# Kernel optimization log

Hardware: AMD Instinct MI355X
Metric: run time of the kernel (lower is better)

Reference implementation:

```python
import jax, jax.numpy as jnp
import numpy as np

HEAD_DIM = 64
CLIP = 64  # clipping_distance
B, S = 32, 1024


def setup_inputs() -> dict:
    key = jax.random.key(0)
    kq, kk, kv, km, kt = jax.random.split(key, 5)
    q = jax.random.normal(kq, (B, S, HEAD_DIM), dtype=jnp.float32)
    k = jax.random.normal(kk, (B, S, HEAD_DIM), dtype=jnp.float32)
    v = jax.random.normal(kv, (B, S, HEAD_DIM), dtype=jnp.float32)
    mask = jax.random.randint(km, (B, S, S), 0, 2).astype(jnp.bool_)
    pos_table = jax.random.normal(kt, (2 * CLIP + 1, HEAD_DIM), dtype=jnp.float32)
    return {"q": q, "k": k, "v": v, "mask": mask, "pos_table": pos_table}


def reference(q, k, v, mask, pos_table):
    scaling = 1.0 / np.sqrt(HEAD_DIM).astype(np.float32)
    Sq, Sk = q.shape[1], k.shape[1]
    # relative positions k_idx - q_idx, clipped to [-CLIP, CLIP]
    rel = jnp.arange(Sk)[None, :] - jnp.arange(Sq)[:, None]      # [Sq, Sk]
    idx = jnp.clip(rel, -CLIP, CLIP) + CLIP                      # [Sq, Sk]
    pe = pos_table[idx]                                          # [Sq, Sk, D]
    # content logits + relative positional logits
    logits = jnp.einsum('bqd,bkd->bqk', q, k) + jnp.einsum('bqd,qkd->bqk', q, pe)
    logits = logits * scaling
    logits = jnp.where(mask, -jnp.inf, logits)
    attn = jax.nn.softmax(logits, axis=-1)                       # [B, Sq, Sk]
    return jnp.einsum('bqk,bkd->bqd', attn, v)
```

## Files before the change

### kernel.cpp

```cpp
#include <hip/hip_runtime.h>
#include <stdint.h>

#define BATCH 32
#define SEQ   1024
#define DIM   64
#define NKT   (SEQ / 64)

typedef uint16_t u16;
typedef uint32_t u32;
typedef __attribute__((ext_vector_type(8))) __bf16 bf16x8;
typedef __attribute__((ext_vector_type(4))) float  f32x4;
typedef __attribute__((ext_vector_type(4))) u32    u32x4;

__device__ __forceinline__ u16 f2bf(float f) {
    u32 x = __builtin_bit_cast(u32, f);
    x += 0x7FFFu + ((x >> 16) & 1u);
    return (u16)(x >> 16);
}

__device__ __forceinline__ bf16x8 cvt8(const float* __restrict__ p) {
    f32x4 a = *reinterpret_cast<const f32x4*>(p);
    f32x4 b = *reinterpret_cast<const f32x4*>(p + 4);
    u16 t[8];
    t[0] = f2bf(a[0]); t[1] = f2bf(a[1]); t[2] = f2bf(a[2]); t[3] = f2bf(a[3]);
    t[4] = f2bf(b[0]); t[5] = f2bf(b[1]); t[6] = f2bf(b[2]); t[7] = f2bf(b[3]);
    return __builtin_bit_cast(bf16x8, *reinterpret_cast<u32x4*>(t));
}

__device__ __forceinline__ bf16x8 ldg8(const u16* p) {
    u32x4 u = *reinterpret_cast<const u32x4*>(p);
    return __builtin_bit_cast(bf16x8, u);
}

__global__ __launch_bounds__(256) void vt_kernel(const float* __restrict__ v,
                                                 u16* __restrict__ vt) {
    __shared__ u16 tile[64][72];
    const int b  = blockIdx.y;
    const int k0 = blockIdx.x * 64;
    const int t  = threadIdx.x;
    const float* vb  = v  + (size_t)b * SEQ * DIM;
    u16*         vtb = vt + (size_t)b * DIM * SEQ;

    {
        int kk = t >> 2;
        int d0 = (t & 3) * 16;
        const float* src = vb + (size_t)(k0 + kk) * DIM + d0;
        u16 tmp[16];
#pragma unroll
        for (int i = 0; i < 4; ++i) {
            f32x4 a = *reinterpret_cast<const f32x4*>(src + i * 4);
            tmp[i * 4 + 0] = f2bf(a[0]); tmp[i * 4 + 1] = f2bf(a[1]);
            tmp[i * 4 + 2] = f2bf(a[2]); tmp[i * 4 + 3] = f2bf(a[3]);
        }
        *reinterpret_cast<u32x4*>(&tile[kk][d0])     = *reinterpret_cast<u32x4*>(tmp);
        *reinterpret_cast<u32x4*>(&tile[kk][d0 + 8]) = *reinterpret_cast<u32x4*>(tmp + 8);
    }
    __syncthreads();
#pragma unroll
    for (int i = 0; i < 2; ++i) {
        int d  = t / 8 + i * 32;
        int ks = (t % 8) * 8;
        u16 tmp[8];
#pragma unroll
        for (int j = 0; j < 8; ++j) tmp[j] = tile[ks + j][d];
        *reinterpret_cast<u32x4*>(vtb + (size_t)d * SEQ + k0 + ks) =
            *reinterpret_cast<u32x4*>(tmp);
    }
}

template <bool USE_VT>
__global__ __launch_bounds__(256, 2) void attn_kernel(
    const float* __restrict__ qg, const float* __restrict__ kg,
    const void* __restrict__ vgv, const int* __restrict__ maskg,
    const float* __restrict__ ptg, float* __restrict__ outg) {
    __shared__ float qp[64][132];
    __shared__ int   mlds[4][16][68];
    __shared__ u16   plds[4][16][72];

    const int b    = blockIdx.y;
    const int q0   = blockIdx.x * 64;
    const int tid  = threadIdx.x;
    const int wave = tid >> 6;
    const int lane = tid & 63;
    const int quad = lane >> 4;
    const int c16  = lane & 15;

    const float* qb = qg + ((size_t)b * SEQ + q0) * DIM;
    const float* kb = kg + (size_t)b * SEQ * DIM;
    const int*   mb = maskg + ((size_t)b * SEQ + q0) * SEQ;

    const bf16x8 qA0 = cvt8(qb + (size_t)(wave * 16 + c16) * DIM + quad * 8);
    const bf16x8 qA1 = cvt8(qb + (size_t)(wave * 16 + c16) * DIM + 32 + quad * 8);

    for (int jt = 0; jt < 9; ++jt) {
        int j0 = jt * 16;
        int jr = min(j0 + c16, 128);
        bf16x8 b0 = cvt8(ptg + (size_t)jr * DIM + quad * 8);
        bf16x8 b1 = cvt8(ptg + (size_t)jr * DIM + 32 + quad * 8);
        f32x4 acc = {0.f, 0.f, 0.f, 0.f};
        acc = __builtin_amdgcn_mfma_f32_16x16x32_bf16(qA0, b0, acc, 0, 0, 0);
        acc = __builtin_amdgcn_mfma_f32_16x16x32_bf16(qA1, b1, acc, 0, 0, 0);
        int jcol = j0 + c16;
        if (jcol <= 128) {
#pragma unroll
            for (int r = 0; r < 4; ++r)
                qp[wave * 16 + quad * 4 + r][jcol] = acc[r];
        }
    }

    float m_run[4], l_run[4];
    f32x4 O[4];
#pragma unroll
    for (int r = 0; r < 4; ++r) { m_run[r] = -1e30f; l_run[r] = 0.f; }
#pragma unroll
    for (int d = 0; d < 4; ++d) O[d] = f32x4{0.f, 0.f, 0.f, 0.f};

#pragma unroll 1
    for (int kt = 0; kt < NKT; ++kt) {
        const int k0 = kt * 64;

        {
            int row_l = lane >> 2;
            const int* mrow = mb + (size_t)(wave * 16 + row_l) * SEQ + k0;
#pragma unroll
            for (int i = 0; i < 4; ++i) {
                int seg = (lane & 3) + i * 4;
                *reinterpret_cast<u32x4*>(&mlds[wave][row_l][seg * 4]) =
                    *reinterpret_cast<const u32x4*>(mrow + seg * 4);
            }
        }

        f32x4 S[4];
#pragma unroll
        for (int sub = 0; sub < 4; ++sub) {
            const float* kr = kb + (size_t)(k0 + sub * 16 + c16) * DIM;
            bf16x8 kb0 = cvt8(kr + quad * 8);
            bf16x8 kb1 = cvt8(kr + 32 + quad * 8);
            f32x4 acc = {0.f, 0.f, 0.f, 0.f};
            acc = __builtin_amdgcn_mfma_f32_16x16x32_bf16(qA0, kb0, acc, 0, 0, 0);
            acc = __builtin_amdgcn_mfma_f32_16x16x32_bf16(qA1, kb1, acc, 0, 0, 0);
            S[sub] = acc;
        }

        float sv[4][4];
#pragma unroll
        for (int sub = 0; sub < 4; ++sub) {
#pragma unroll
            for (int r = 0; r < 4; ++r) {
                int row_l = quad * 4 + r;
                int row_g = q0 + wave * 16 + row_l;
                int col_g = k0 + sub * 16 + c16;
                int rel = col_g - row_g;
                rel = rel < -64 ? -64 : (rel > 64 ? 64 : rel);
                float x = (S[sub][r] + qp[wave * 16 + row_l][rel + 64]) * 0.125f;
                int mv = mlds[wave][row_l][sub * 16 + c16];
                sv[sub][r] = mv ? -1e30f : x;
            }
        }

        float m_new[4], alpha[4];
#pragma unroll
        for (int r = 0; r < 4; ++r) {
            float rmax = fmaxf(fmaxf(sv[0][r], sv[1][r]), fmaxf(sv[2][r], sv[3][r]));
            rmax = fmaxf(rmax, __shfl_xor(rmax, 1));
            rmax = fmaxf(rmax, __shfl_xor(rmax, 2));
            rmax = fmaxf(rmax, __shfl_xor(rmax, 4));
            rmax = fmaxf(rmax, __shfl_xor(rmax, 8));
            m_new[r] = fmaxf(m_run[r], rmax);
            alpha[r] = __expf(m_run[r] - m_new[r]);
            m_run[r] = m_new[r];
        }
#pragma unroll
        for (int r = 0; r < 4; ++r) {
            float rs = 0.f;
#pragma unroll
            for (int sub = 0; sub < 4; ++sub) {
                float e = __expf(sv[sub][r] - m_new[r]);
                rs += e;
                plds[wave][quad * 4 + r][sub * 16 + c16] = f2bf(e);
            }
            rs += __shfl_xor(rs, 1);
            rs += __shfl_xor(rs, 2);
            rs += __shfl_xor(rs, 4);
            rs += __shfl_xor(rs, 8);
            l_run[r] = l_run[r] * alpha[r] + rs;
#pragma unroll
            for (int d = 0; d < 4; ++d) O[d][r] *= alpha[r];
        }

        bf16x8 pA0 = *reinterpret_cast<bf16x8*>(&plds[wave][c16][quad * 8]);
        bf16x8 pA1 = *reinterpret_cast<bf16x8*>(&plds[wave][c16][32 + quad * 8]);
#pragma unroll
        for (int d = 0; d < 4; ++d) {
            bf16x8 vb0, vb1;
            if (USE_VT) {
                const u16* vtb = (const u16*)vgv + (size_t)b * DIM * SEQ +
                                 (size_t)(d * 16 + c16) * SEQ + k0;
                vb0 = ldg8(vtb + quad * 8);
                vb1 = ldg8(vtb + 32 + quad * 8);
            } else {
                u16 t0[8], t1[8];
                const float* vbase = (const float*)vgv +
                                     ((size_t)b * SEQ + k0) * DIM + d * 16 + c16;
#pragma unroll
                for (int j = 0; j < 8; ++j) {
                    t0[j] = f2bf(vbase[(size_t)(quad * 8 + j) * DIM]);
                    t1[j] = f2bf(vbase[(size_t)(32 + quad * 8 + j) * DIM]);
                }
                vb0 = __builtin_bit_cast(bf16x8, *reinterpret_cast<u32x4*>(t0));
                vb1 = __builtin_bit_cast(bf16x8, *reinterpret_cast<u32x4*>(t1));
            }
            O[d] = __builtin_amdgcn_mfma_f32_16x16x32_bf16(pA0, vb0, O[d], 0, 0, 0);
            O[d] = __builtin_amdgcn_mfma_f32_16x16x32_bf16(pA1, vb1, O[d], 0, 0, 0);
        }
    }

    float* ob = outg + ((size_t)b * SEQ + q0) * DIM;
#pragma unroll
    for (int r = 0; r < 4; ++r) {
        float inv = 1.f / l_run[r];
        int row_l = wave * 16 + quad * 4 + r;
#pragma unroll
        for (int d = 0; d < 4; ++d)
            ob[(size_t)row_l * DIM + d * 16 + c16] = O[d][r] * inv;
    }
}

extern "C" void kernel_launch(void* const* d_in, const int* in_sizes, int n_in,
                              void* d_out, int out_size, void* d_ws, size_t ws_size,
                              hipStream_t stream) {
    const float* q    = (const float*)d_in[0];
    const float* k    = (const float*)d_in[1];
    const float* v    = (const float*)d_in[2];
    const int*   mask = (const int*)d_in[3];
    const float* pt   = (const float*)d_in[4];
    float* out        = (float*)d_out;

    const size_t vt_bytes = (size_t)BATCH * SEQ * DIM * sizeof(u16);
    dim3 grid(SEQ / 64, BATCH);

    if (ws_size >= vt_bytes) {
        u16* vt = (u16*)d_ws;
        vt_kernel<<<grid, 256, 0, stream>>>(v, vt);
        attn_kernel<true><<<grid, 256, 0, stream>>>(q, k, (const void*)vt, mask, pt, out);
    } else {
        attn_kernel<false><<<grid, 256, 0, stream>>>(q, k, (const void*)v, mask, pt, out);
    }
}
```

Baseline: 274.3 us.

## Prepack mask to bits and K to bf16, add exp2-based fast attention kernel

Adds preprocessing kernels that convert K to bf16 and pack the int32 mask into one bit per element. A new attention kernel reads these compact forms instead of converting K on every tile and staging the mask through shared memory. It also folds the softmax scale and log2(e) into Q so it can use exp2, prefetches the next tile's mask words, and raises occupancy to 3 blocks per CU. The cost is two extra launches and a full pass over the 128MB mask in the packing kernel, which is still timed, so the gain relies on not re-reading the int32 mask in the main loop.

After: 287.5 us. 1.05x slower.

```diff
diff --git a/kernel.cpp b/kernel.cpp
--- a/kernel.cpp
+++ b/kernel.cpp
@@ -8,9 +8,18 @@
 
 typedef uint16_t u16;
 typedef uint32_t u32;
+typedef unsigned long long u64;
 typedef __attribute__((ext_vector_type(8))) __bf16 bf16x8;
 typedef __attribute__((ext_vector_type(4))) float  f32x4;
 typedef __attribute__((ext_vector_type(4))) u32    u32x4;
+
+__device__ __forceinline__ float fexp2(float x) {
+#if __has_builtin(__builtin_amdgcn_exp2f)
+    return __builtin_amdgcn_exp2f(x);
+#else
+    return exp2f(x);
+#endif
+}
 
 __device__ __forceinline__ u16 f2bf(float f) {
     u32 x = __builtin_bit_cast(u32, f);
@@ -27,9 +36,27 @@
     return __builtin_bit_cast(bf16x8, *reinterpret_cast<u32x4*>(t));
 }
 
+__device__ __forceinline__ bf16x8 cvt8s(const float* __restrict__ p, float s) {
+    f32x4 a = *reinterpret_cast<const f32x4*>(p);
+    f32x4 b = *reinterpret_cast<const f32x4*>(p + 4);
+    u16 t[8];
+    t[0] = f2bf(a[0] * s); t[1] = f2bf(a[1] * s); t[2] = f2bf(a[2] * s); t[3] = f2bf(a[3] * s);
+    t[4] = f2bf(b[0] * s); t[5] = f2bf(b[1] * s); t[6] = f2bf(b[2] * s); t[7] = f2bf(b[3] * s);
+    return __builtin_bit_cast(bf16x8, *reinterpret_cast<u32x4*>(t));
+}
+
 __device__ __forceinline__ bf16x8 ldg8(const u16* p) {
     u32x4 u = *reinterpret_cast<const u32x4*>(p);
     return __builtin_bit_cast(bf16x8, u);
+}
+
+__device__ __forceinline__ u64 spread4(u64 x) {
+    x &= 0xFFFFull;
+    x = (x | (x << 24)) & 0x000000FF000000FFull;
+    x = (x | (x << 12)) & 0x000F000F000F000Full;
+    x = (x | (x << 6))  & 0x0303030303030303ull;
+    x = (x | (x << 3))  & 0x1111111111111111ull;
+    return x;
 }
 
 __global__ __launch_bounds__(256) void vt_kernel(const float* __restrict__ v,
@@ -68,13 +95,43 @@
     }
 }
 
-template <bool USE_VT>
-__global__ __launch_bounds__(256, 2) void attn_kernel(
-    const float* __restrict__ qg, const float* __restrict__ kg,
-    const void* __restrict__ vgv, const int* __restrict__ maskg,
+__global__ __launch_bounds__(256) void kbf_kernel(const float* __restrict__ k,
+                                                  u16* __restrict__ kb) {
+    size_t i = ((size_t)blockIdx.x * 256 + threadIdx.x) * 8;
+    bf16x8 v = cvt8(k + i);
+    *reinterpret_cast<u32x4*>(kb + i) = __builtin_bit_cast(u32x4, v);
+}
+
+__global__ __launch_bounds__(256) void mpack_kernel(const int* __restrict__ m,
+                                                    u64* __restrict__ bits) {
+    const int wid  = blockIdx.x * 4 + (threadIdx.x >> 6);
+    const int lane = threadIdx.x & 63;
+#pragma unroll 1
+    for (int it = 0; it < 16; ++it) {
+        size_t g = (size_t)wid + (size_t)it * 8192;
+        const int* p = m + g * 256 + lane * 4;
+        u32x4 x = *reinterpret_cast<const u32x4*>(p);
+        int nib = (x[0] != 0) | ((x[1] != 0) << 1) | ((x[2] != 0) << 2) | ((x[3] != 0) << 3);
+        u64 b0 = __ballot(nib & 1);
+        u64 b1 = __ballot(nib & 2);
+        u64 b2 = __ballot(nib & 4);
+        u64 b3 = __ballot(nib & 8);
+        if (lane < 4) {
+            int sh = lane * 16;
+            u64 w = spread4(b0 >> sh)
+                  | (spread4(b1 >> sh) << 1)
+                  | (spread4(b2 >> sh) << 2)
+                  | (spread4(b3 >> sh) << 3);
+            bits[g * 4 + lane] = w;
+        }
+    }
+}
+
+__global__ __launch_bounds__(256, 3) void attn_fast(
+    const float* __restrict__ qg, const u16* __restrict__ kbf,
+    const u16* __restrict__ vt, const u64* __restrict__ mbits,
     const float* __restrict__ ptg, float* __restrict__ outg) {
     __shared__ float qp[64][132];
-    __shared__ int   mlds[4][16][68];
     __shared__ u16   plds[4][16][72];
 
     const int b    = blockIdx.y;
@@ -85,12 +142,12 @@
     const int quad = lane >> 4;
     const int c16  = lane & 15;
 
+    const float SC = 0.125f * 1.44269504088896340736f;
+
     const float* qb = qg + ((size_t)b * SEQ + q0) * DIM;
-    const float* kb = kg + (size_t)b * SEQ * DIM;
-    const int*   mb = maskg + ((size_t)b * SEQ + q0) * SEQ;
-
-    const bf16x8 qA0 = cvt8(qb + (size_t)(wave * 16 + c16) * DIM + quad * 8);
-    const bf16x8 qA1 = cvt8(qb + (size_t)(wave * 16 + c16) * DIM + 32 + quad * 8);
+
+    const bf16x8 qA0 = cvt8s(qb + (size_t)(wave * 16 + c16) * DIM + quad * 8, SC);
+    const bf16x8 qA1 = cvt8s(qb + (size_t)(wave * 16 + c16) * DIM + 32 + quad * 8, SC);
 
     for (int jt = 0; jt < 9; ++jt) {
         int j0 = jt * 16;
@@ -108,6 +165,14 @@
         }
     }
 
+    const u16* kb_base  = kbf + (size_t)b * SEQ * DIM;
+    const u16* vtb_base = vt  + (size_t)b * DIM * SEQ;
+    const u64* mrow     = mbits + (size_t)(b * SEQ + q0 + wave * 16) * NKT;
+
+    u64 w[4];
+#pragma unroll
+    for (int r = 0; r < 4; ++r) w[r] = mrow[(quad * 4 + r) * NKT];
+
     float m_run[4], l_run[4];
     f32x4 O[4];
 #pragma unroll
@@ -119,6 +184,146 @@
     for (int kt = 0; kt < NKT; ++kt) {
         const int k0 = kt * 64;
 
+        u64 wn[4];
+        const int ktn = (kt + 1) & (NKT - 1);
+#pragma unroll
+        for (int r = 0; r < 4; ++r) wn[r] = mrow[(quad * 4 + r) * NKT + ktn];
+
+        f32x4 S[4];
+#pragma unroll
+        for (int sub = 0; sub < 4; ++sub) {
+            const u16* kr = kb_base + (size_t)(k0 + sub * 16 + c16) * DIM;
+            bf16x8 kf0 = ldg8(kr + quad * 8);
+            bf16x8 kf1 = ldg8(kr + 32 + quad * 8);
+            f32x4 acc = {0.f, 0.f, 0.f, 0.f};
+            acc = __builtin_amdgcn_mfma_f32_16x16x32_bf16(qA0, kf0, acc, 0, 0, 0);
+            acc = __builtin_amdgcn_mfma_f32_16x16x32_bf16(qA1, kf1, acc, 0, 0, 0);
+            S[sub] = acc;
+        }
+
+        float sv[4][4];
+#pragma unroll
+        for (int r = 0; r < 4; ++r) {
+            const int row_l = quad * 4 + r;
+            const int row_g = q0 + wave * 16 + row_l;
+            const u64 wr = w[r] >> c16;
+#pragma unroll
+            for (int sub = 0; sub < 4; ++sub) {
+                int col_g = k0 + sub * 16 + c16;
+                int rel = col_g - row_g;
+                rel = rel < -64 ? -64 : (rel > 64 ? 64 : rel);
+                float x = S[sub][r] + qp[wave * 16 + row_l][rel + 64];
+                u32 bit = (u32)(wr >> (sub * 16)) & 1u;
+                sv[sub][r] = bit ? -1e30f : x;
+            }
+        }
+
+        float m_new[4], alpha[4];
+#pragma unroll
+        for (int r = 0; r < 4; ++r) {
+            float rmax = fmaxf(fmaxf(sv[0][r], sv[1][r]), fmaxf(sv[2][r], sv[3][r]));
+            rmax = fmaxf(rmax, __shfl_xor(rmax, 1));
+            rmax = fmaxf(rmax, __shfl_xor(rmax, 2));
+            rmax = fmaxf(rmax, __shfl_xor(rmax, 4));
+            rmax = fmaxf(rmax, __shfl_xor(rmax, 8));
+            m_new[r] = fmaxf(m_run[r], rmax);
+            alpha[r] = fexp2(m_run[r] - m_new[r]);
+            m_run[r] = m_new[r];
+        }
+#pragma unroll
+        for (int r = 0; r < 4; ++r) {
+            float rs = 0.f;
+#pragma unroll
+            for (int sub = 0; sub < 4; ++sub) {
+                float e = fexp2(sv[sub][r] - m_new[r]);
+                rs += e;
+                plds[wave][quad * 4 + r][sub * 16 + c16] = f2bf(e);
+            }
+            rs += __shfl_xor(rs, 1);
+            rs += __shfl_xor(rs, 2);
+            rs += __shfl_xor(rs, 4);
+            rs += __shfl_xor(rs, 8);
+            l_run[r] = l_run[r] * alpha[r] + rs;
+#pragma unroll
+            for (int d = 0; d < 4; ++d) O[d][r] *= alpha[r];
+        }
+
+        bf16x8 pA0 = *reinterpret_cast<bf16x8*>(&plds[wave][c16][quad * 8]);
+        bf16x8 pA1 = *reinterpret_cast<bf16x8*>(&plds[wave][c16][32 + quad * 8]);
+#pragma unroll
+        for (int d = 0; d < 4; ++d) {
+            const u16* vr = vtb_base + (size_t)(d * 16 + c16) * SEQ + k0;
+            bf16x8 vf0 = ldg8(vr + quad * 8);
+            bf16x8 vf1 = ldg8(vr + 32 + quad * 8);
+            O[d] = __builtin_amdgcn_mfma_f32_16x16x32_bf16(pA0, vf0, O[d], 0, 0, 0);
+            O[d] = __builtin_amdgcn_mfma_f32_16x16x32_bf16(pA1, vf1, O[d], 0, 0, 0);
+        }
+
+#pragma unroll
+        for (int r = 0; r < 4; ++r) w[r] = wn[r];
+    }
+
+    float* ob = outg + ((size_t)b * SEQ + q0) * DIM;
+#pragma unroll
+    for (int r = 0; r < 4; ++r) {
+        float inv = 1.f / l_run[r];
+        int row_l = wave * 16 + quad * 4 + r;
+#pragma unroll
+        for (int d = 0; d < 4; ++d)
+            ob[(size_t)row_l * DIM + d * 16 + c16] = O[d][r] * inv;
+    }
+}
+
+template <bool USE_VT>
+__global__ __launch_bounds__(256, 2) void attn_kernel(
+    const float* __restrict__ qg, const float* __restrict__ kg,
+    const void* __restrict__ vgv, const int* __restrict__ maskg,
+    const float* __restrict__ ptg, float* __restrict__ outg) {
+    __shared__ float qp[64][132];
+    __shared__ int   mlds[4][16][68];
+    __shared__ u16   plds[4][16][72];
+
+    const int b    = blockIdx.y;
+    const int q0   = blockIdx.x * 64;
+    const int tid  = threadIdx.x;
+    const int wave = tid >> 6;
+    const int lane = tid & 63;
+    const int quad = lane >> 4;
+    const int c16  = lane & 15;
+
+    const float* qb = qg + ((size_t)b * SEQ + q0) * DIM;
+    const float* kb = kg + (size_t)b * SEQ * DIM;
+    const int*   mb = maskg + ((size_t)b * SEQ + q0) * SEQ;
+
+    const bf16x8 qA0 = cvt8(qb + (size_t)(wave * 16 + c16) * DIM + quad * 8);
+    const bf16x8 qA1 = cvt8(qb + (size_t)(wave * 16 + c16) * DIM + 32 + quad * 8);
+
+    for (int jt = 0; jt < 9; ++jt) {
+        int j0 = jt * 16;
+        int jr = min(j0 + c16, 128);
+        bf16x8 b0 = cvt8(ptg + (size_t)jr * DIM + quad * 8);
+        bf16x8 b1 = cvt8(ptg + (size_t)jr * DIM + 32 + quad * 8);
+        f32x4 acc = {0.f, 0.f, 0.f, 0.f};
+        acc = __builtin_amdgcn_mfma_f32_16x16x32_bf16(qA0, b0, acc, 0, 0, 0);
+        acc = __builtin_amdgcn_mfma_f32_16x16x32_bf16(qA1, b1, acc, 0, 0, 0);
+        int jcol = j0 + c16;
+        if (jcol <= 128) {
+#pragma unroll
+            for (int r = 0; r < 4; ++r)
+                qp[wave * 16 + quad * 4 + r][jcol] = acc[r];
+        }
+    }
+
+    float m_run[4], l_run[4];
+    f32x4 O[4];
+#pragma unroll
+    for (int r = 0; r < 4; ++r) { m_run[r] = -1e30f; l_run[r] = 0.f; }
+#pragma unroll
+    for (int d = 0; d < 4; ++d) O[d] = f32x4{0.f, 0.f, 0.f, 0.f};
+
+#pragma unroll 1
+    for (int kt = 0; kt < NKT; ++kt) {
+        const int k0 = kt * 64;
         {
             int row_l = lane >> 2;
             const int* mrow = mb + (size_t)(wave * 16 + row_l) * SEQ + k0;
@@ -237,9 +442,19 @@
     float* out        = (float*)d_out;
 
     const size_t vt_bytes = (size_t)BATCH * SEQ * DIM * sizeof(u16);
+    const size_t kb_bytes = (size_t)BATCH * SEQ * DIM * sizeof(u16);
+    const size_t mb_bytes = (size_t)BATCH * SEQ * NKT * sizeof(u64);
     dim3 grid(SEQ / 64, BATCH);
 
-    if (ws_size >= vt_bytes) {
+    if (ws_size >= vt_bytes + kb_bytes + mb_bytes) {
+        u16* vt = (u16*)d_ws;
+        u16* kb = (u16*)((char*)d_ws + vt_bytes);
+        u64* mb2 = (u64*)((char*)d_ws + vt_bytes + kb_bytes);
+        vt_kernel<<<grid, 256, 0, stream>>>(v, vt);
+        kbf_kernel<<<dim3((BATCH * SEQ * DIM / 8) / 256), 256, 0, stream>>>(k, kb);
+        mpack_kernel<<<dim3(2048), 256, 0, stream>>>(mask, mb2);
+        attn_fast<<<grid, 256, 0, stream>>>(q, kb, vt, mb2, pt, out);
+    } else if (ws_size >= vt_bytes) {
         u16* vt = (u16*)d_ws;
         vt_kernel<<<grid, 256, 0, stream>>>(v, vt);
         attn_kernel<true><<<grid, 256, 0, stream>>>(q, k, (const void*)vt, mask, pt, out);
```
